# Kernel tuning notes

Hardware: AMD Instinct MI355X
Metric: run time of the kernel (lower is better)

The kernel has to match this reference:

```python
import jax, jax.numpy as jnp
import numpy as np

D_MODEL, D_INNER, D_STATE, D_CONV, DT_RANK = 512, 1024, 64, 4, 32
B, L = 2, 1000
EPS = 1e-5


def _rmsnorm(x, w):
    return x * jax.lax.rsqrt(jnp.mean(x * x, axis=-1, keepdims=True) + EPS) * w


def _causal_dwconv(x, w, b):
    # x: (B, L, Di); w: (Di, K) depthwise causal conv, output length L
    xT = jnp.transpose(x, (0, 2, 1))  # (B, Di, L)
    y = jax.lax.conv_general_dilated(
        xT, w[:, None, :], window_strides=(1,), padding=[(D_CONV - 1, 0)],
        dimension_numbers=('NCH', 'OIH', 'NCH'), feature_group_count=D_INNER)
    return jnp.transpose(y + b[None, :, None], (0, 2, 1))


def _selective_scan(u, dt, A, Bm, Cm):
    # u, dt: (B, L, Di); A: (Di, N); Bm, Cm: (B, L, N)
    def step(h, inp):
        dt_t, B_t, C_t, u_t = inp
        dA = jnp.exp(dt_t[..., None] * A)                       # (B, Di, N)
        h = dA * h + (dt_t * u_t)[..., None] * B_t[:, None, :]  # state update
        y = jnp.einsum('bdn,bn->bd', h, C_t)
        return h, y
    xs = (jnp.swapaxes(dt, 0, 1), jnp.swapaxes(Bm, 0, 1),
          jnp.swapaxes(Cm, 0, 1), jnp.swapaxes(u, 0, 1))
    h0 = jnp.zeros((u.shape[0], D_INNER, D_STATE), u.dtype)
    _, ys = jax.lax.scan(step, h0, xs)
    return jnp.swapaxes(ys, 0, 1)  # (B, L, Di)


def _mamba_layer(x, norm_w, in_proj, conv_w, conv_b, x_proj, dt_w, dt_b, A_log, Dp, out_proj):
    # mamba-ssm Block with fused_add_norm=False, n_layer=1:
    # residual = x; h = mixer(rmsnorm(x)); block output pair merges to h + x
    h = _rmsnorm(x, norm_w)
    xz = jnp.einsum('bld,ed->ble', h, in_proj)        # (B, L, 2*Di)
    xc, z = jnp.split(xz, 2, axis=-1)
    xc = jax.nn.silu(_causal_dwconv(xc, conv_w, conv_b))
    x_dbl = jnp.einsum('bld,ed->ble', xc, x_proj)     # (B, L, dt_rank + 2N)
    dt, Bm, Cm = jnp.split(x_dbl, [DT_RANK, DT_RANK + D_STATE], axis=-1)
    dt = jax.nn.softplus(jnp.einsum('blr,dr->bld', dt, dt_w) + dt_b)
    A = -jnp.exp(A_log)
    y = _selective_scan(xc, dt, A, Bm, Cm)
    y = (y + xc * Dp) * jax.nn.silu(z)
    return jnp.einsum('bld,ed->ble', y, out_proj) + x


def _forward(x,
             f_norm_w, f_in_proj, f_conv_w, f_conv_b, f_x_proj, f_dt_w, f_dt_b, f_A_log, f_D, f_out_proj,
             b_norm_w, b_in_proj, b_conv_w, b_conv_b, b_x_proj, b_dt_w, b_dt_b, b_A_log, b_D, b_out_proj):
    res_f = _mamba_layer(x, f_norm_w, f_in_proj, f_conv_w, f_conv_b, f_x_proj,
                         f_dt_w, f_dt_b, f_A_log, f_D, f_out_proj)
    res_b = _mamba_layer(jnp.flip(x, 1), b_norm_w, b_in_proj, b_conv_w, b_conv_b,
                         b_x_proj, b_dt_w, b_dt_b, b_A_log, b_D, b_out_proj)
    return res_f + jnp.flip(res_b, 1)  # bidirectional_merging='add'


def setup_inputs() -> dict:
    key = jax.random.key(0)
    ks = iter(jax.random.split(key, 32))
    def nrm(shape, s=0.02):
        return jax.random.normal(next(ks), shape, jnp.float32) * s
    inp = {'x': jax.random.normal(next(ks), (B, L, D_MODEL), jnp.float32)}
    for p in ('f', 'b'):
        inp[p + '_norm_w'] = jnp.ones((D_MODEL,), jnp.float32)
        inp[p + '_in_proj'] = nrm((2 * D_INNER, D_MODEL))
        inp[p + '_conv_w'] = nrm((D_INNER, D_CONV), 0.1)
        inp[p + '_conv_b'] = nrm((D_INNER,), 0.1)
        inp[p + '_x_proj'] = nrm((DT_RANK + 2 * D_STATE, D_INNER))
        inp[p + '_dt_w'] = nrm((D_INNER, DT_RANK), 0.1)
        inp[p + '_dt_b'] = jnp.full((D_INNER,), float(np.log(np.expm1(0.01))), jnp.float32)
        inp[p + '_A_log'] = jnp.log(jnp.tile(jnp.arange(1, D_STATE + 1, dtype=jnp.float32), (D_INNER, 1)))
        inp[p + '_D'] = jnp.ones((D_INNER,), jnp.float32)
        inp[p + '_out_proj'] = nrm((D_MODEL, D_INNER))
    return inp


def reference(x,
              f_norm_w, f_in_proj, f_conv_w, f_conv_b, f_x_proj, f_dt_w, f_dt_b, f_A_log, f_D, f_out_proj,
              b_norm_w, b_in_proj, b_conv_w, b_conv_b, b_x_proj, b_dt_w, b_dt_b, b_A_log, b_D, b_out_proj):
    return _forward(x,
                    f_norm_w, f_in_proj, f_conv_w, f_conv_b, f_x_proj, f_dt_w, f_dt_b, f_A_log, f_D, f_out_proj,
                    b_norm_w, b_in_proj, b_conv_w, b_conv_b, b_x_proj, b_dt_w, b_dt_b, b_A_log, b_D, b_out_proj)
```

## Files before the change

kernel.cpp:

```cpp
#include <hip/hip_runtime.h>
#include <hip/hip_bf16.h>
#include <math.h>

#define DM   512
#define DI   1024
#define NS   64
#define RDT  32
#define BB   2
#define LL   1000
#define MROWS (BB*LL)

typedef __attribute__((ext_vector_type(8))) short bf16x8;
typedef __attribute__((ext_vector_type(4))) float f32x4;

__device__ __forceinline__ unsigned short f2bf(float f) {
    unsigned u = __builtin_bit_cast(unsigned, f);
    u = (u + 0x7FFF + ((u >> 16) & 1)) >> 16;
    return (unsigned short)u;
}
__device__ __forceinline__ float bf2f(unsigned short h) {
    unsigned u = (unsigned)h << 16;
    return __builtin_bit_cast(float, u);
}
__device__ __forceinline__ float bcast_lane(float v, int lane) {
    return __builtin_bit_cast(float,
        __builtin_amdgcn_readlane(__builtin_bit_cast(int, v), lane));
}

__global__ __launch_bounds__(256)
void rmsnorm_k(const float* __restrict__ x,
               const float* __restrict__ nw0, const float* __restrict__ nw1,
               unsigned short* __restrict__ xnb0, unsigned short* __restrict__ xnb1) {
    int row = blockIdx.x;
    int tid = threadIdx.x;
    const float* xr = x + (size_t)row * DM;
    float2 v = *(const float2*)(xr + tid * 2);
    float ss = v.x * v.x + v.y * v.y;
    #pragma unroll
    for (int off = 32; off; off >>= 1) ss += __shfl_xor(ss, off, 64);
    __shared__ float red[4];
    if ((tid & 63) == 0) red[tid >> 6] = ss;
    __syncthreads();
    float tot = red[0] + red[1] + red[2] + red[3];
    float scale = rsqrtf(tot / (float)DM + 1e-5f);
    float2 w0 = *(const float2*)(nw0 + tid * 2);
    float2 w1 = *(const float2*)(nw1 + tid * 2);
    short2 o0, o1;
    o0.x = (short)f2bf(v.x * scale * w0.x);
    o0.y = (short)f2bf(v.y * scale * w0.y);
    o1.x = (short)f2bf(v.x * scale * w1.x);
    o1.y = (short)f2bf(v.y * scale * w1.y);
    *(short2*)(xnb0 + (size_t)row * DM + tid * 2) = o0;
    *(short2*)(xnb1 + (size_t)row * DM + tid * 2) = o1;
}

__global__ __launch_bounds__(256)
void cvt2_k(const float* __restrict__ in0, const float* __restrict__ in1,
            unsigned short* __restrict__ out0, unsigned short* __restrict__ out1,
            int n4) {
    int idx = blockIdx.x * 256 + threadIdx.x;
    if (idx >= n4) return;
    const float* in = blockIdx.y ? in1 : in0;
    unsigned short* out = blockIdx.y ? out1 : out0;
    float4 v = *(const float4*)(in + (size_t)idx * 4);
    short4 o;
    o.x = (short)f2bf(v.x); o.y = (short)f2bf(v.y);
    o.z = (short)f2bf(v.z); o.w = (short)f2bf(v.w);
    *(short4*)(out + (size_t)idx * 4) = o;
}

__global__ __launch_bounds__(256, 2)
void gemm1_mfma(const unsigned short* __restrict__ xnb0,
                const unsigned short* __restrict__ xnb1,
                const unsigned short* __restrict__ wib0,
                const unsigned short* __restrict__ wib1,
                unsigned short* __restrict__ xzb0, unsigned short* __restrict__ xzb1)
{
    __shared__ __align__(16) unsigned short As[128 * 40];
    __shared__ __align__(16) unsigned short Bs[128 * 40];
    int dir = blockIdx.z;
    const unsigned short* A = dir ? xnb1 : xnb0;
    const unsigned short* W = dir ? wib1 : wib0;
    unsigned short* C = dir ? xzb1 : xzb0;
    int n0 = blockIdx.x * 128, m0 = blockIdx.y * 128;
    int tid = threadIdx.x;
    int wv = tid >> 6, lane = tid & 63;
    int wr = wv >> 1, wc = wv & 1;
    int fl = lane & 15, kg = lane >> 4;

    f32x4 acc[4][4];
    #pragma unroll
    for (int i = 0; i < 4; i++)
        #pragma unroll
        for (int j = 0; j < 4; j++) acc[i][j] = (f32x4){0.f, 0.f, 0.f, 0.f};

    int sr = tid >> 2, cg = tid & 3;
    for (int k0 = 0; k0 < 512; k0 += 32) {
        #pragma unroll
        for (int i = 0; i < 2; i++) {
            int row = sr + i * 64;
            int m = m0 + row;
            float4 av = make_float4(0.f, 0.f, 0.f, 0.f);
            if (m < MROWS) {
                int rs = m;
                if (dir) { int b = m / LL, t = m % LL; rs = b * LL + (LL - 1 - t); }
                av = *(const float4*)(A + (size_t)rs * 512 + k0 + cg * 8);
            }
            *(float4*)(&As[row * 40 + cg * 8]) = av;
            float4 wv4 = *(const float4*)(W + (size_t)(n0 + row) * 512 + k0 + cg * 8);
            *(float4*)(&Bs[row * 40 + cg * 8]) = wv4;
        }
        __syncthreads();
        bf16x8 af[4], bf[4];
        #pragma unroll
        for (int fr = 0; fr < 4; fr++)
            af[fr] = *(const bf16x8*)(&As[(wr * 64 + fr * 16 + fl) * 40 + kg * 8]);
        #pragma unroll
        for (int fc = 0; fc < 4; fc++)
            bf[fc] = *(const bf16x8*)(&Bs[(wc * 64 + fc * 16 + fl) * 40 + kg * 8]);
        #pragma unroll
        for (int fr = 0; fr < 4; fr++)
            #pragma unroll
            for (int fc = 0; fc < 4; fc++)
                acc[fr][fc] = __builtin_amdgcn_mfma_f32_16x16x32_bf16(
                    af[fr], bf[fc], acc[fr][fc], 0, 0, 0);
        __syncthreads();
    }
    #pragma unroll
    for (int fr = 0; fr < 4; fr++)
        #pragma unroll
        for (int fc = 0; fc < 4; fc++)
            #pragma unroll
            for (int j = 0; j < 4; j++) {
                int m = m0 + wr * 64 + fr * 16 + kg * 4 + j;
                if (m < MROWS) {
                    int n = n0 + wc * 64 + fc * 16 + fl;
                    C[(size_t)m * 2048 + n] = f2bf(acc[fr][fc][j]);
                }
            }
}

__global__ __launch_bounds__(256, 2)
void gemm_out_mfma(const unsigned short* __restrict__ ygb0,
                   const unsigned short* __restrict__ ygb1,
                   const unsigned short* __restrict__ wob0,
                   const unsigned short* __restrict__ wob1,
                   float* __restrict__ partial)
{
    __shared__ __align__(16) unsigned short As[128 * 40];
    __shared__ __align__(16) unsigned short Bs[128 * 40];
    int dir = blockIdx.z;
    const unsigned short* A = dir ? ygb1 : ygb0;
    const unsigned short* W = dir ? wob1 : wob0;
    float* P = partial + (size_t)dir * MROWS * 512;
    int n0 = blockIdx.x * 128, m0 = blockIdx.y * 128;
    int tid = threadIdx.x;
    int wv = tid >> 6, lane = tid & 63;
    int wr = wv >> 1, wc = wv & 1;
    int fl = lane & 15, kg = lane >> 4;

    f32x4 acc[4][4];
    #pragma unroll
    for (int i = 0; i < 4; i++)
        #pragma unroll
        for (int j = 0; j < 4; j++) acc[i][j] = (f32x4){0.f, 0.f, 0.f, 0.f};

    int sr = tid >> 2, cg = tid & 3;
    for (int k0 = 0; k0 < 1024; k0 += 32) {
        #pragma unroll
        for (int i = 0; i < 2; i++) {
            int row = sr + i * 64;
            int m = m0 + row;
            float4 av = make_float4(0.f, 0.f, 0.f, 0.f);
            if (m < MROWS)
                av = *(const float4*)(A + (size_t)m * 1024 + k0 + cg * 8);
            *(float4*)(&As[row * 40 + cg * 8]) = av;
            float4 wv4 = *(const float4*)(W + (size_t)(n0 + sr + i * 64) * 1024 + k0 + cg * 8);
            *(float4*)(&Bs[row * 40 + cg * 8]) = wv4;
        }
        __syncthreads();
        bf16x8 af[4], bf[4];
        #pragma unroll
        for (int fr = 0; fr < 4; fr++)
            af[fr] = *(const bf16x8*)(&As[(wr * 64 + fr * 16 + fl) * 40 + kg * 8]);
        #pragma unroll
        for (int fc = 0; fc < 4; fc++)
            bf[fc] = *(const bf16x8*)(&Bs[(wc * 64 + fc * 16 + fl) * 40 + kg * 8]);
        #pragma unroll
        for (int fr = 0; fr < 4; fr++)
            #pragma unroll
            for (int fc = 0; fc < 4; fc++)
                acc[fr][fc] = __builtin_amdgcn_mfma_f32_16x16x32_bf16(
                    af[fr], bf[fc], acc[fr][fc], 0, 0, 0);
        __syncthreads();
    }
    #pragma unroll
    for (int fr = 0; fr < 4; fr++)
        #pragma unroll
        for (int fc = 0; fc < 4; fc++)
            #pragma unroll
            for (int j = 0; j < 4; j++) {
                int m = m0 + wr * 64 + fr * 16 + kg * 4 + j;
                if (m < MROWS) {
                    int n = n0 + wc * 64 + fc * 16 + fl;
                    P[(size_t)m * 512 + n] = acc[fr][fc][j];
                }
            }
}

__global__ __launch_bounds__(256)
void reduce_out_k(const float* __restrict__ x, const float* __restrict__ partial,
                  float* __restrict__ out)
{
    int idx = blockIdx.x * 256 + threadIdx.x;
    if (idx >= MROWS * 128) return;
    int m = idx >> 7, q = idx & 127;
    int b = m / LL, t = m % LL;
    int fm = b * LL + (LL - 1 - t);
    const float* p0 = partial;
    const float* p1 = partial + (size_t)MROWS * 512;
    float4 xv = *(const float4*)(x  + (size_t)m  * 512 + q * 4);
    float4 a  = *(const float4*)(p0 + (size_t)m  * 512 + q * 4);
    float4 c  = *(const float4*)(p1 + (size_t)fm * 512 + q * 4);
    float4 o;
    o.x = 2.f * xv.x + a.x + c.x;
    o.y = 2.f * xv.y + a.y + c.y;
    o.z = 2.f * xv.z + a.z + c.z;
    o.w = 2.f * xv.w + a.w + c.w;
    *(float4*)(out + (size_t)m * 512 + q * 4) = o;
}

__global__ __launch_bounds__(256)
void conv_silu_k(const unsigned short* __restrict__ xzb0,
                 const unsigned short* __restrict__ xzb1,
                 const float* __restrict__ cw0, const float* __restrict__ cw1,
                 const float* __restrict__ cb0, const float* __restrict__ cb1,
                 float* __restrict__ xcT0, float* __restrict__ xcT1,
                 unsigned short* __restrict__ xcb0, unsigned short* __restrict__ xcb1)
{
    __shared__ float Ls[64 * 65];
    int dirb = blockIdx.z;
    int dir = dirb >> 1, b = dirb & 1;
    int d0 = blockIdx.x * 64, t0 = blockIdx.y * 64;
    int tid = threadIdx.x;
    int dl = tid & 63, tg = tid >> 6;

    const unsigned short* in = (dir ? xzb1 : xzb0) + (size_t)b * LL * 2048;
    const float* cw = dir ? cw1 : cw0;
    const float* cb = dir ? cb1 : cb0;
    float*      xcT = dir ? xcT1 : xcT0;
    unsigned short* xcb = dir ? xcb1 : xcb0;

    float4 w4 = ((const float4*)cw)[d0 + dl];
    float bias = cb[d0 + dl];

    int ts = t0 + tg * 16;
    float x3 = 0.f, x2 = 0.f, x1 = 0.f;
    if (ts - 3 >= 0 && ts - 3 < LL) x3 = bf2f(in[(size_t)(ts - 3) * 2048 + d0 + dl]);
    if (ts - 2 >= 0 && ts - 2 < LL) x2 = bf2f(in[(size_t)(ts - 2) * 2048 + d0 + dl]);
    if (ts - 1 >= 0 && ts - 1 < LL) x1 = bf2f(in[(size_t)(ts - 1) * 2048 + d0 + dl]);

    #pragma unroll
    for (int i = 0; i < 16; i++) {
        int t = ts + i;
        float x0v = (t < LL) ? bf2f(in[(size_t)t * 2048 + d0 + dl]) : 0.f;
        float a = bias + x3 * w4.x + x2 * w4.y + x1 * w4.z + x0v * w4.w;
        float s = a / (1.f + __expf(-a));
        Ls[dl * 65 + tg * 16 + i] = s;
        if (t < LL)
            xcb[((size_t)(b * LL + t)) * 1024 + d0 + dl] = f2bf(s);
        x3 = x2; x2 = x1; x1 = x0v;
    }
    __syncthreads();
    int tl = tid & 63, dg = tid >> 6;
    #pragma unroll
    for (int i = 0; i < 16; i++) {
        int dd = dg * 16 + i;
        int t = t0 + tl;
        if (t < LL)
            xcT[((size_t)(b * 1024) + d0 + dd) * LL + t] = Ls[dd * 65 + tl];
    }
}

__global__ __launch_bounds__(256, 2)
void gemm_xp_mfma(const unsigned short* __restrict__ xcb0,
                  const unsigned short* __restrict__ xcb1,
                  const unsigned short* __restrict__ xpb0,
                  const unsigned short* __restrict__ xpb1,
                  float* __restrict__ xd0, float* __restrict__ xd1,
                  float* __restrict__ bct)
{
    __shared__ __align__(16) unsigned short As[64 * 40];
    __shared__ __align__(16) unsigned short Ws[160 * 40];
    int dirb = blockIdx.y;
    int dir = dirb >> 1, b = dirb & 1;
    const unsigned short* A = (dir ? xcb1 : xcb0) + (size_t)b * LL * 1024;
    const unsigned short* W = dir ? xpb1 : xpb0;
    float* xd = (dir ? xd1 : xd0) + (size_t)b * LL * 32;
    float* bc = bct + (size_t)dirb * 128 * LL;
    int m0 = blockIdx.x * 64;
    int tid = threadIdx.x;
    int wv = tid >> 6, lane = tid & 63;
    int fl = lane & 15, kg = lane >> 4;

    f32x4 acc[10];
    #pragma unroll
    for (int f = 0; f < 10; f++) acc[f] = (f32x4){0.f, 0.f, 0.f, 0.f};

    int sr = tid >> 2, cg = tid & 3;
    for (int k0 = 0; k0 < 1024; k0 += 32) {
        {
            int t = m0 + sr;
            float4 av = make_float4(0.f, 0.f, 0.f, 0.f);
            if (t < LL)
                av = *(const float4*)(A + (size_t)t * 1024 + k0 + cg * 8);
            *(float4*)(&As[sr * 40 + cg * 8]) = av;
        }
        #pragma unroll
        for (int it = 0; it < 3; it++) {
            int row = sr + it * 64;
            if (row < 160) {
                float4 wv4 = *(const float4*)(W + (size_t)row * 1024 + k0 + cg * 8);
                *(float4*)(&Ws[row * 40 + cg * 8]) = wv4;
            }
        }
        __syncthreads();
        bf16x8 af = *(const bf16x8*)(&As[(wv * 16 + fl) * 40 + kg * 8]);
        #pragma unroll
        for (int f = 0; f < 10; f++) {
            bf16x8 bf = *(const bf16x8*)(&Ws[(f * 16 + fl) * 40 + kg * 8]);
            acc[f] = __builtin_amdgcn_mfma_f32_16x16x32_bf16(af, bf, acc[f], 0, 0, 0);
        }
        __syncthreads();
    }

    #pragma unroll
    for (int f = 0; f < 10; f++) {
        int n = f * 16 + fl;
        #pragma unroll
        for (int j = 0; j < 4; j++) {
            int t = m0 + wv * 16 + kg * 4 + j;
            if (t >= LL) continue;
            if (f < 2) xd[(size_t)t * 32 + n] = acc[f][j];
            else       bc[(size_t)(n - 32) * LL + t] = acc[f][j];
        }
    }
}

__global__ __launch_bounds__(256)
void gemm_dt_k(const float* __restrict__ xd0, const float* __restrict__ xd1,
               const float* __restrict__ w0, const float* __restrict__ w1,
               const float* __restrict__ bb0, const float* __restrict__ bb1,
               float* __restrict__ dtT0, float* __restrict__ dtT1)
{
    __shared__ float As[64 * 33];
    __shared__ float Ws[32 * 68];
    __shared__ float T[64 * 67];
    int dirb = blockIdx.z;
    int dir = dirb >> 1, b = dirb & 1;
    const float* xd = (dir ? xd1 : xd0) + (size_t)b * LL * 32;
    const float* W  = dir ? w1 : w0;
    const float* bi = dir ? bb1 : bb0;
    float*      dtT = (dir ? dtT1 : dtT0) + (size_t)b * 1024 * LL;
    int n0 = blockIdx.x * 64, t0 = blockIdx.y * 64;
    int tid = threadIdx.x;
    int tx = tid & 15, ty = tid >> 4;

    #pragma unroll
    for (int i = 0; i < 2; i++) {
        int j = tid + 256 * i;
        int row = j >> 3, q = j & 7;
        float4 v = make_float4(0.f, 0.f, 0.f, 0.f);
        if (t0 + row < LL)
            v = *(const float4*)(xd + (size_t)(t0 + row) * 32 + (q & 7) * 4);
        As[row * 33 + q * 4 + 0] = v.x;
        As[row * 33 + q * 4 + 1] = v.y;
        As[row * 33 + q * 4 + 2] = v.z;
        As[row * 33 + q * 4 + 3] = v.w;
        float4 wv = *(const float4*)(W + (size_t)(n0 + row) * 32 + q * 4);
        Ws[(q * 4 + 0) * 68 + row] = wv.x;
        Ws[(q * 4 + 1) * 68 + row] = wv.y;
        Ws[(q * 4 + 2) * 68 + row] = wv.z;
        Ws[(q * 4 + 3) * 68 + row] = wv.w;
    }
    __syncthreads();

    float acc[4][4] = {};
    #pragma unroll 8
    for (int k = 0; k < 32; k++) {
        float4 w = *(const float4*)(Ws + k * 68 + tx * 4);
        float wvv[4] = {w.x, w.y, w.z, w.w};
        float av[4];
        #pragma unroll
        for (int i = 0; i < 4; i++) av[i] = As[(ty * 4 + i) * 33 + k];
        #pragma unroll
        for (int i = 0; i < 4; i++)
            #pragma unroll
            for (int j = 0; j < 4; j++)
                acc[i][j] = fmaf(av[i], wvv[j], acc[i][j]);
    }
    __syncthreads();

    #pragma unroll
    for (int i = 0; i < 4; i++) {
        #pragma unroll
        for (int j = 0; j < 4; j++) {
            int n = tx * 4 + j;
            float v = acc[i][j] + bi[n0 + n];
            v = (v > 20.f) ? v : log1pf(__expf(v));
            T[n * 67 + ty * 4 + i] = v;
        }
    }
    __syncthreads();

    int tl = tid & 63, ng = tid >> 6;
    #pragma unroll
    for (int i = 0; i < 16; i++) {
        int nl = ng * 16 + i;
        int t = t0 + tl;
        if (t < LL)
            dtT[(size_t)(n0 + nl) * LL + t] = T[nl * 67 + tl];
    }
}

__global__ __launch_bounds__(256)
void scan_k(float* __restrict__ dtT0, float* __restrict__ dtT1,
            const float* __restrict__ ucT0, const float* __restrict__ ucT1,
            const float* __restrict__ bct,
            const float* __restrict__ Al0, const float* __restrict__ Al1,
            const float* __restrict__ Dc0, const float* __restrict__ Dc1)
{
    __shared__ float Bs[64 * 34];
    __shared__ float Cs[64 * 34];
    __shared__ float Pt[4][16 * 66];
    int dirb = blockIdx.y;
    int dir = dirb >> 1, b = dirb & 1;
    int wid = threadIdx.x >> 6, lane = threadIdx.x & 63;
    int d = blockIdx.x * 4 + wid;
    float* Pw = Pt[wid];

    float*       dtT = (dir ? dtT1 : dtT0);
    const float* ucT = (dir ? ucT1 : ucT0);
    const float* Al  = dir ? Al1 : Al0;
    const float* Dc  = dir ? Dc1 : Dc0;

    float a  = -__expf(Al[d * 64 + lane]) * 1.44269504f;
    float Dp = Dc[d];
    float h  = 0.f;
    size_t chan = ((size_t)(b * 1024 + d)) * LL;
    const float* Bg = bct + (size_t)dirb * 128 * LL;

    int srow = threadIdx.x >> 2;
    int scol = (threadIdx.x & 3) * 8;
    int tl16 = lane & 15, qq = lane >> 4;
    const float* Prow = Pw + tl16 * 66 + qq * 16;

    float4 rb0, rb1, rc0, rc1;
    float dta = 0.f, ua = 0.f;
    {
        const float* Bp = Bg + (size_t)srow * LL + scol;
        const float* Cp = Bg + (size_t)(srow + 64) * LL + scol;
        rb0 = *(const float4*)(Bp);     rb1 = *(const float4*)(Bp + 4);
        rc0 = *(const float4*)(Cp);     rc1 = *(const float4*)(Cp + 4);
        if (lane < 32) {
            dta = dtT[chan + lane];
            ua  = ucT[chan + lane];
        }
    }

    for (int t0 = 0; t0 < LL; t0 += 32) {
        int rem = min(32, LL - t0);
        __syncthreads();
        *(float4*)(&Bs[srow * 34 + scol])     = rb0;
        *(float4*)(&Bs[srow * 34 + scol + 4]) = rb1;
        *(float4*)(&Cs[srow * 34 + scol])     = rc0;
        *(float4*)(&Cs[srow * 34 + scol + 4]) = rc1;
        float dcur = dta, ucur = ua;
        float wsc  = dcur * ucur;
        __syncthreads();

        if (t0 + 32 < LL) {
            const float* Bp = Bg + (size_t)srow * LL + (t0 + 32) + scol;
            const float* Cp = Bg + (size_t)(srow + 64) * LL + (t0 + 32) + scol;
            rb0 = *(const float4*)(Bp);     rb1 = *(const float4*)(Bp + 4);
            rc0 = *(const float4*)(Cp);     rc1 = *(const float4*)(Cp + 4);
            if (lane < min(32, LL - t0 - 32)) {
                dta = dtT[chan + t0 + 32 + lane];
                ua  = ucT[chan + t0 + 32 + lane];
            }
        }

        for (int sec = 0; sec < 2; sec++) {
            int sbase = sec * 16;
            int steps = rem - sbase;
            if (steps <= 0) break;
            if (steps > 16) steps = 16;
            if (steps < 16) {
                for (int i = steps; i < 16; i++) Pw[i * 66 + lane] = 0.f;
            }
            int ngr = (steps + 7) >> 3;
            for (int g = 0; g < ngr; g++) {
                int tb = sbase + g * 8;
                float4 B0 = *(const float4*)(&Bs[lane * 34 + tb]);
                float4 B1 = *(const float4*)(&Bs[lane * 34 + tb + 4]);
                float4 C0 = *(const float4*)(&Cs[lane * 34 + tb]);
                float4 C1 = *(const float4*)(&Cs[lane * 34 + tb + 4]);
                #pragma unroll
                for (int i = 0; i < 8; i++) {
                    float dtv = bcast_lane(dcur, tb + i);
                    float w   = bcast_lane(wsc,  tb + i);
                    float dA  = exp2f(dtv * a);
                    float Bn  = (i < 4) ? B0[i] : B1[i - 4];
                    float Cn  = (i < 4) ? C0[i] : C1[i - 4];
                    h = fmaf(dA, h, w * Bn);
                    Pw[(g * 8 + i) * 66 + lane] = h * Cn;
                }
            }
            float s = 0.f;
            #pragma unroll
            for (int j = 0; j < 8; j++) {
                float2 v = *(const float2*)(Prow + j * 2);
                s += v.x + v.y;
            }
#if __has_builtin(__builtin_amdgcn_permlane32_swap)
            {
                unsigned aa = __builtin_bit_cast(unsigned, s);
                auto r = __builtin_amdgcn_permlane32_swap(aa, aa, false, false);
                s = __builtin_bit_cast(float, (unsigned)r[0]) +
                    __builtin_bit_cast(float, (unsigned)r[1]);
            }
#else
            s += __shfl_xor(s, 32, 64);
#endif
#if __has_builtin(__builtin_amdgcn_permlane16_swap)
            {
                unsigned aa = __builtin_bit_cast(unsigned, s);
                auto r = __builtin_amdgcn_permlane16_swap(aa, aa, false, false);
                s = __builtin_bit_cast(float, (unsigned)r[0]) +
                    __builtin_bit_cast(float, (unsigned)r[1]);
            }
#else
            s += __shfl_xor(s, 16, 64);
#endif
            float uf = __shfl(ucur, sbase + tl16, 64);
            s = fmaf(uf, Dp, s);
            if (lane < steps)
                dtT[chan + t0 + sbase + lane] = s;
        }
    }
}

__global__ __launch_bounds__(256)
void gate_k(const float* __restrict__ yT0, const float* __restrict__ yT1,
            const unsigned short* __restrict__ xzb0,
            const unsigned short* __restrict__ xzb1,
            unsigned short* __restrict__ yg0, unsigned short* __restrict__ yg1)
{
    __shared__ float Ls[64 * 65];
    int dirb = blockIdx.z;
    int dir = dirb >> 1, b = dirb & 1;
    int d0 = blockIdx.x * 64, t0 = blockIdx.y * 64;
    int tid = threadIdx.x;
    const float* yT = (dir ? yT1 : yT0) + (size_t)b * 1024 * LL;
    const unsigned short* xz = (dir ? xzb1 : xzb0) + (size_t)b * LL * 2048;
    unsigned short* yg = dir ? yg1 : yg0;

    int tl = tid & 63, dg = tid >> 6;
    #pragma unroll
    for (int i = 0; i < 16; i++) {
        int dd = dg * 16 + i;
        int t = t0 + tl;
        float v = (t < LL) ? yT[(size_t)(d0 + dd) * LL + t] : 0.f;
        Ls[dd * 65 + tl] = v;
    }
    __syncthreads();
    int dcol = tid & 63, tg = tid >> 6;
    #pragma unroll
    for (int i = 0; i < 16; i++) {
        int t = t0 + tg * 16 + i;
        if (t >= LL) continue;
        float z = bf2f(xz[(size_t)t * 2048 + 1024 + d0 + dcol]);
        float y = Ls[dcol * 65 + tg * 16 + i];
        float s = z / (1.f + __expf(-z));
        yg[((size_t)(b * LL + t)) * 1024 + d0 + dcol] = f2bf(y * s);
    }
}

extern "C" void kernel_launch(void* const* d_in, const int* in_sizes, int n_in,
                              void* d_out, int out_size, void* d_ws, size_t ws_size,
                              hipStream_t stream) {
    const float* x = (const float*)d_in[0];
    const float* P[2][10];
    for (int dir = 0; dir < 2; dir++)
        for (int i = 0; i < 10; i++)
            P[dir][i] = (const float*)d_in[1 + dir * 10 + i];

    float* ws = (float*)d_ws;
    unsigned short* xzb0 = (unsigned short*)(ws);
    unsigned short* xzb1 = (unsigned short*)(ws + 4096000);
    float* xcT0  = ws + 8192000;
    float* xcT1  = ws + 10240000;
    float* dtT0  = ws + 12288000;
    float* dtT1  = ws + 14336000;
    float* xdbl0 = ws + 16384000;
    float* xdbl1 = ws + 16448000;
    unsigned short* xnb0 = (unsigned short*)(ws + 17024000);
    unsigned short* xnb1 = (unsigned short*)(ws + 17280000);
    unsigned short* wib0 = (unsigned short*)(ws + 14336000);
    unsigned short* wib1 = (unsigned short*)(ws + 14860288);
    unsigned short* xcb0 = (unsigned short*)(ws + 12288000);
    unsigned short* xcb1 = (unsigned short*)(ws + 13312000);
    unsigned short* xpb0 = (unsigned short*)(ws + 17024000);
    unsigned short* xpb1 = (unsigned short*)(ws + 17280000);
    unsigned short* ygb0 = (unsigned short*)xcT0;
    unsigned short* ygb1 = (unsigned short*)xcT1;
    unsigned short* wob0 = (unsigned short*)dtT0;
    unsigned short* wob1 = (unsigned short*)(dtT0 + 262144);
    float* partial = ws;
    float* bct = (float*)d_out;
    float* out = (float*)d_out;

    rmsnorm_k<<<MROWS, 256, 0, stream>>>(x, P[0][0], P[1][0], xnb0, xnb1);

    cvt2_k<<<dim3(1024, 2), 256, 0, stream>>>(P[0][1], P[1][1], wib0, wib1, 262144);

    gemm1_mfma<<<dim3(16, 16, 2), 256, 0, stream>>>(
        xnb0, xnb1, wib0, wib1, xzb0, xzb1);

    cvt2_k<<<dim3(160, 2), 256, 0, stream>>>(P[0][4], P[1][4], xpb0, xpb1, 40960);

    conv_silu_k<<<dim3(16, 16, 4), 256, 0, stream>>>(
        xzb0, xzb1, P[0][2], P[1][2], P[0][3], P[1][3], xcT0, xcT1, xcb0, xcb1);

    gemm_xp_mfma<<<dim3(16, 4), 256, 0, stream>>>(
        xcb0, xcb1, xpb0, xpb1, xdbl0, xdbl1, bct);

    gemm_dt_k<<<dim3(16, 16, 4), 256, 0, stream>>>(
        xdbl0, xdbl1, P[0][5], P[1][5], P[0][6], P[1][6], dtT0, dtT1);

    scan_k<<<dim3(256, 4), 256, 0, stream>>>(
        dtT0, dtT1, xcT0, xcT1, bct,
        P[0][7], P[1][7], P[0][8], P[1][8]);

    gate_k<<<dim3(16, 16, 4), 256, 0, stream>>>(
        dtT0, dtT1, xzb0, xzb1, ygb0, ygb1);

    cvt2_k<<<dim3(512, 2), 256, 0, stream>>>(P[0][9], P[1][9], wob0, wob1, 131072);

    gemm_out_mfma<<<dim3(4, 16, 2), 256, 0, stream>>>(
        ygb0, ygb1, wob0, wob1, partial);

    reduce_out_k<<<1000, 256, 0, stream>>>(x, partial, out);
}
```

Measured before the change: 296.5 us.

## Fuse weight bf16 conversion into GEMM loaders and use DPP reductions in scan

Removes the three separate fp32-to-bf16 weight conversion kernels and instead converts weights on the fly while staging them into shared memory inside each GEMM. This drops three launches and their global round-trips, but each GEMM tile now reads fp32 weights, twice the bytes, repeatedly across M-blocks. The scan kernel also replaces its 64-wide shared-memory partial-sum transpose and permlane reductions with DPP row adds across groups of 4 lanes and a smaller shared buffer, cutting LDS traffic in the inner loop.

```diff
diff --git a/kernel.cpp b/kernel.cpp
--- a/kernel.cpp
+++ b/kernel.cpp
@@ -25,6 +25,24 @@
 __device__ __forceinline__ float bcast_lane(float v, int lane) {
     return __builtin_bit_cast(float,
         __builtin_amdgcn_readlane(__builtin_bit_cast(int, v), lane));
+}
+__device__ __forceinline__ void cvt8_st(const float* __restrict__ src,
+                                        unsigned short* dst) {
+    float4 a0 = *(const float4*)(src);
+    float4 a1 = *(const float4*)(src + 4);
+    short4 o0, o1;
+    o0.x = (short)f2bf(a0.x); o0.y = (short)f2bf(a0.y);
+    o0.z = (short)f2bf(a0.z); o0.w = (short)f2bf(a0.w);
+    o1.x = (short)f2bf(a1.x); o1.y = (short)f2bf(a1.y);
+    o1.z = (short)f2bf(a1.z); o1.w = (short)f2bf(a1.w);
+    *(short4*)(dst)     = o0;
+    *(short4*)(dst + 4) = o1;
+}
+template<int CTRL>
+__device__ __forceinline__ float dpp_add(float v) {
+    int iv = __builtin_bit_cast(int, v);
+    int mv = __builtin_amdgcn_update_dpp(iv, iv, CTRL, 0xf, 0xf, false);
+    return v + __builtin_bit_cast(float, mv);
 }
 
 __global__ __launch_bounds__(256)
@@ -54,33 +72,17 @@
     *(short2*)(xnb1 + (size_t)row * DM + tid * 2) = o1;
 }
 
-__global__ __launch_bounds__(256)
-void cvt2_k(const float* __restrict__ in0, const float* __restrict__ in1,
-            unsigned short* __restrict__ out0, unsigned short* __restrict__ out1,
-            int n4) {
-    int idx = blockIdx.x * 256 + threadIdx.x;
-    if (idx >= n4) return;
-    const float* in = blockIdx.y ? in1 : in0;
-    unsigned short* out = blockIdx.y ? out1 : out0;
-    float4 v = *(const float4*)(in + (size_t)idx * 4);
-    short4 o;
-    o.x = (short)f2bf(v.x); o.y = (short)f2bf(v.y);
-    o.z = (short)f2bf(v.z); o.w = (short)f2bf(v.w);
-    *(short4*)(out + (size_t)idx * 4) = o;
-}
-
 __global__ __launch_bounds__(256, 2)
 void gemm1_mfma(const unsigned short* __restrict__ xnb0,
                 const unsigned short* __restrict__ xnb1,
-                const unsigned short* __restrict__ wib0,
-                const unsigned short* __restrict__ wib1,
+                const float* __restrict__ wi0, const float* __restrict__ wi1,
                 unsigned short* __restrict__ xzb0, unsigned short* __restrict__ xzb1)
 {
     __shared__ __align__(16) unsigned short As[128 * 40];
     __shared__ __align__(16) unsigned short Bs[128 * 40];
     int dir = blockIdx.z;
     const unsigned short* A = dir ? xnb1 : xnb0;
-    const unsigned short* W = dir ? wib1 : wib0;
+    const float* W = dir ? wi1 : wi0;
     unsigned short* C = dir ? xzb1 : xzb0;
     int n0 = blockIdx.x * 128, m0 = blockIdx.y * 128;
     int tid = threadIdx.x;
@@ -107,8 +109,8 @@
                 av = *(const float4*)(A + (size_t)rs * 512 + k0 + cg * 8);
             }
             *(float4*)(&As[row * 40 + cg * 8]) = av;
-            float4 wv4 = *(const float4*)(W + (size_t)(n0 + row) * 512 + k0 + cg * 8);
-            *(float4*)(&Bs[row * 40 + cg * 8]) = wv4;
+            cvt8_st(W + (size_t)(n0 + row) * 512 + k0 + cg * 8,
+                    &Bs[row * 40 + cg * 8]);
         }
         __syncthreads();
         bf16x8 af[4], bf[4];
@@ -143,15 +145,14 @@
 __global__ __launch_bounds__(256, 2)
 void gemm_out_mfma(const unsigned short* __restrict__ ygb0,
                    const unsigned short* __restrict__ ygb1,
-                   const unsigned short* __restrict__ wob0,
-                   const unsigned short* __restrict__ wob1,
+                   const float* __restrict__ wo0, const float* __restrict__ wo1,
                    float* __restrict__ partial)
 {
     __shared__ __align__(16) unsigned short As[128 * 40];
     __shared__ __align__(16) unsigned short Bs[128 * 40];
     int dir = blockIdx.z;
     const unsigned short* A = dir ? ygb1 : ygb0;
-    const unsigned short* W = dir ? wob1 : wob0;
+    const float* W = dir ? wo1 : wo0;
     float* P = partial + (size_t)dir * MROWS * 512;
     int n0 = blockIdx.x * 128, m0 = blockIdx.y * 128;
     int tid = threadIdx.x;
@@ -175,8 +176,8 @@
             if (m < MROWS)
                 av = *(const float4*)(A + (size_t)m * 1024 + k0 + cg * 8);
             *(float4*)(&As[row * 40 + cg * 8]) = av;
-            float4 wv4 = *(const float4*)(W + (size_t)(n0 + sr + i * 64) * 1024 + k0 + cg * 8);
-            *(float4*)(&Bs[row * 40 + cg * 8]) = wv4;
+            cvt8_st(W + (size_t)(n0 + row) * 1024 + k0 + cg * 8,
+                    &Bs[row * 40 + cg * 8]);
         }
         __syncthreads();
         bf16x8 af[4], bf[4];
@@ -285,8 +286,7 @@
 __global__ __launch_bounds__(256, 2)
 void gemm_xp_mfma(const unsigned short* __restrict__ xcb0,
                   const unsigned short* __restrict__ xcb1,
-                  const unsigned short* __restrict__ xpb0,
-                  const unsigned short* __restrict__ xpb1,
+                  const float* __restrict__ xp0, const float* __restrict__ xp1,
                   float* __restrict__ xd0, float* __restrict__ xd1,
                   float* __restrict__ bct)
 {
@@ -295,7 +295,7 @@
     int dirb = blockIdx.y;
     int dir = dirb >> 1, b = dirb & 1;
     const unsigned short* A = (dir ? xcb1 : xcb0) + (size_t)b * LL * 1024;
-    const unsigned short* W = dir ? xpb1 : xpb0;
+    const float* W = dir ? xp1 : xp0;
     float* xd = (dir ? xd1 : xd0) + (size_t)b * LL * 32;
     float* bc = bct + (size_t)dirb * 128 * LL;
     int m0 = blockIdx.x * 64;
@@ -319,10 +319,9 @@
         #pragma unroll
         for (int it = 0; it < 3; it++) {
             int row = sr + it * 64;
-            if (row < 160) {
-                float4 wv4 = *(const float4*)(W + (size_t)row * 1024 + k0 + cg * 8);
-                *(float4*)(&Ws[row * 40 + cg * 8]) = wv4;
-            }
+            if (row < 160)
+                cvt8_st(W + (size_t)row * 1024 + k0 + cg * 8,
+                        &Ws[row * 40 + cg * 8]);
         }
         __syncthreads();
         bf16x8 af = *(const bf16x8*)(&As[(wv * 16 + fl) * 40 + kg * 8]);
@@ -432,12 +431,12 @@
 {
     __shared__ float Bs[64 * 34];
     __shared__ float Cs[64 * 34];
-    __shared__ float Pt[4][16 * 66];
+    __shared__ __align__(16) float Pq[4][16 * 24];
     int dirb = blockIdx.y;
     int dir = dirb >> 1, b = dirb & 1;
     int wid = threadIdx.x >> 6, lane = threadIdx.x & 63;
     int d = blockIdx.x * 4 + wid;
-    float* Pw = Pt[wid];
+    float* Pw = Pq[wid];
 
     float*       dtT = (dir ? dtT1 : dtT0);
     const float* ucT = (dir ? ucT1 : ucT0);
@@ -452,8 +451,7 @@
 
     int srow = threadIdx.x >> 2;
     int scol = (threadIdx.x & 3) * 8;
-    int tl16 = lane & 15, qq = lane >> 4;
-    const float* Prow = Pw + tl16 * 66 + qq * 16;
+    int tloc = lane >> 2, qd = lane & 3;
 
     float4 rb0, rb1, rc0, rc1;
     float dta = 0.f, ua = 0.f;
@@ -495,9 +493,6 @@
             int steps = rem - sbase;
             if (steps <= 0) break;
             if (steps > 16) steps = 16;
-            if (steps < 16) {
-                for (int i = steps; i < 16; i++) Pw[i * 66 + lane] = 0.f;
-            }
             int ngr = (steps + 7) >> 3;
             for (int g = 0; g < ngr; g++) {
                 int tb = sbase + g * 8;
@@ -513,39 +508,21 @@
                     float Bn  = (i < 4) ? B0[i] : B1[i - 4];
                     float Cn  = (i < 4) ? C0[i] : C1[i - 4];
                     h = fmaf(dA, h, w * Bn);
-                    Pw[(g * 8 + i) * 66 + lane] = h * Cn;
+                    float p = h * Cn;
+                    p = dpp_add<0x121>(p);
+                    p = dpp_add<0x122>(p);
+                    if (qd == 0)
+                        Pw[(g * 8 + i) * 24 + tloc] = p;
                 }
             }
-            float s = 0.f;
-            #pragma unroll
-            for (int j = 0; j < 8; j++) {
-                float2 v = *(const float2*)(Prow + j * 2);
-                s += v.x + v.y;
-            }
-#if __has_builtin(__builtin_amdgcn_permlane32_swap)
-            {
-                unsigned aa = __builtin_bit_cast(unsigned, s);
-                auto r = __builtin_amdgcn_permlane32_swap(aa, aa, false, false);
-                s = __builtin_bit_cast(float, (unsigned)r[0]) +
-                    __builtin_bit_cast(float, (unsigned)r[1]);
-            }
-#else
-            s += __shfl_xor(s, 32, 64);
-#endif
-#if __has_builtin(__builtin_amdgcn_permlane16_swap)
-            {
-                unsigned aa = __builtin_bit_cast(unsigned, s);
-                auto r = __builtin_amdgcn_permlane16_swap(aa, aa, false, false);
-                s = __builtin_bit_cast(float, (unsigned)r[0]) +
-                    __builtin_bit_cast(float, (unsigned)r[1]);
-            }
-#else
-            s += __shfl_xor(s, 16, 64);
-#endif
-            float uf = __shfl(ucur, sbase + tl16, 64);
+            float4 v = *(const float4*)(&Pw[tloc * 24 + qd * 4]);
+            float s = (v.x + v.y) + (v.z + v.w);
+            s = dpp_add<0x121>(s);
+            s = dpp_add<0x122>(s);
+            float uf = __shfl(ucur, sbase + tloc, 64);
             s = fmaf(uf, Dp, s);
-            if (lane < steps)
-                dtT[chan + t0 + sbase + lane] = s;
+            if (qd == 0 && tloc < steps)
+                dtT[chan + t0 + sbase + tloc] = s;
         }
     }
 }
@@ -606,34 +583,24 @@
     float* xdbl1 = ws + 16448000;
     unsigned short* xnb0 = (unsigned short*)(ws + 17024000);
     unsigned short* xnb1 = (unsigned short*)(ws + 17280000);
-    unsigned short* wib0 = (unsigned short*)(ws + 14336000);
-    unsigned short* wib1 = (unsigned short*)(ws + 14860288);
     unsigned short* xcb0 = (unsigned short*)(ws + 12288000);
     unsigned short* xcb1 = (unsigned short*)(ws + 13312000);
-    unsigned short* xpb0 = (unsigned short*)(ws + 17024000);
-    unsigned short* xpb1 = (unsigned short*)(ws + 17280000);
     unsigned short* ygb0 = (unsigned short*)xcT0;
     unsigned short* ygb1 = (unsigned short*)xcT1;
-    unsigned short* wob0 = (unsigned short*)dtT0;
-    unsigned short* wob1 = (unsigned short*)(dtT0 + 262144);
     float* partial = ws;
     float* bct = (float*)d_out;
     float* out = (float*)d_out;
 
     rmsnorm_k<<<MROWS, 256, 0, stream>>>(x, P[0][0], P[1][0], xnb0, xnb1);
 
-    cvt2_k<<<dim3(1024, 2), 256, 0, stream>>>(P[0][1], P[1][1], wib0, wib1, 262144);
-
     gemm1_mfma<<<dim3(16, 16, 2), 256, 0, stream>>>(
-        xnb0, xnb1, wib0, wib1, xzb0, xzb1);
-
-    cvt2_k<<<dim3(160, 2), 256, 0, stream>>>(P[0][4], P[1][4], xpb0, xpb1, 40960);
+        xnb0, xnb1, P[0][1], P[1][1], xzb0, xzb1);
 
     conv_silu_k<<<dim3(16, 16, 4), 256, 0, stream>>>(
         xzb0, xzb1, P[0][2], P[1][2], P[0][3], P[1][3], xcT0, xcT1, xcb0, xcb1);
 
     gemm_xp_mfma<<<dim3(16, 4), 256, 0, stream>>>(
-        xcb0, xcb1, xpb0, xpb1, xdbl0, xdbl1, bct);
+        xcb0, xcb1, P[0][4], P[1][4], xdbl0, xdbl1, bct);
 
     gemm_dt_k<<<dim3(16, 16, 4), 256, 0, stream>>>(
         xdbl0, xdbl1, P[0][5], P[1][5], P[0][6], P[1][6], dtT0, dtT1);
@@ -645,10 +612,8 @@
     gate_k<<<dim3(16, 16, 4), 256, 0, stream>>>(
         dtT0, dtT1, xzb0, xzb1, ygb0, ygb1);
 
-    cvt2_k<<<dim3(512, 2), 256, 0, stream>>>(P[0][9], P[1][9], wob0, wob1, 131072);
-
     gemm_out_mfma<<<dim3(4, 16, 2), 256, 0, stream>>>(
-        ygb0, ygb1, wob0, wob1, partial);
+        ygb0, ygb1, P[0][9], P[1][9], partial);
 
     reduce_out_k<<<1000, 256, 0, stream>>>(x, partial, out);
 }
```

After: 357.4 us. +20.6%, slower.
